# Kernel tuning notes

Hardware: AMD Instinct MI355X
Metric: run time of the kernel (lower is better)

The kernel has to match this reference:

```python
import math
import jax, jax.numpy as jnp
import numpy as np

H = 16  # head_count
D = 1024  # model_dim
DH = D // H  # dim_per_head = 64
PAD_IDX = 1


def setup_inputs() -> dict:
    key = jax.random.key(0)
    ks = jax.random.split(key, 16)
    B, L = 4, 512
    s = 0.02
    inp = {
        'key': jax.random.normal(ks[0], (B, L, D), jnp.float32),
        'value': jax.random.normal(ks[1], (B, L, D), jnp.float32),
        'query': jax.random.normal(ks[2], (B, L, D), jnp.float32),
        'ast_parents_matrix': jax.random.randint(ks[3], (B, L, L), 0, 200, jnp.int32),
        'mask': jnp.zeros((B, 1, L), jnp.bool_),
        'Wq': jax.random.normal(ks[4], (D, D), jnp.float32) * s,
        'bq': jnp.zeros((D,), jnp.float32),
        'Wk': jax.random.normal(ks[5], (D, D), jnp.float32) * s,
        'bk': jnp.zeros((D,), jnp.float32),
        'Wv': jax.random.normal(ks[6], (D, D), jnp.float32) * s,
        'bv': jnp.zeros((D,), jnp.float32),
        'Wo': jax.random.normal(ks[7], (D, D), jnp.float32) * s,
        'bo': jnp.zeros((D,), jnp.float32),
        'struct_emb': jax.random.normal(ks[8], (200, DH), jnp.float32).at[PAD_IDX].set(0.0),
        'value_emb': jax.random.normal(ks[9], (10000, DH), jnp.float32).at[PAD_IDX].set(0.0),
    }
    return inp


def _parent_embeddings(matrix, struct_emb, value_emb):
    # matrix: (B, Lq, K) int ids; even key positions use structure vocab, odd use value vocab
    B, Lq, K = matrix.shape
    s_ids = matrix[:, :, ::2]   # (B, Lq, ceil(K/2))
    v_ids = matrix[:, :, 1::2]  # (B, Lq, floor(K/2))
    emb_s = struct_emb[s_ids]   # (B, Lq, S, DH)
    emb_v = value_emb[v_ids]    # (B, Lq, V, DH)
    S = emb_s.shape[2]
    if emb_v.shape[2] != S:  # odd K: pad value stream by one zero slot, drop after interleave
        emb_v = jnp.concatenate([emb_v, jnp.zeros_like(emb_s[:, :, :1])], axis=2)
    pe = jnp.stack([emb_s, emb_v], axis=3).reshape(B, Lq, 2 * S, DH)
    return pe[:, :, :K, :]  # (B, Lq, K, DH)


def reference(key, value, query, ast_parents_matrix, mask,
              Wq, bq, Wk, bk, Wv, bv, Wo, bo, struct_emb, value_emb):
    B, L, _ = query.shape

    def shape(x):
        return x.reshape(B, -1, H, DH).transpose(0, 2, 1, 3)  # (B,H,L,DH)

    q = shape(query @ Wq + bq) / math.sqrt(DH)
    k = shape(key @ Wk + bk)
    v = shape(value @ Wv + bv)

    qk = jnp.einsum('bhid,bhjd->bhij', q, k)  # (B,H,L,L)

    pe = _parent_embeddings(ast_parents_matrix[:, :, :L], struct_emb, value_emb)
    score_ast = jnp.einsum('bhid,bijd->bhij', q, pe)

    scores = (qk + score_ast).astype(jnp.float32)
    scores = jnp.where(mask[:, None, :, :], -1e18, scores)  # mask: (B,1,L)->(B,1,1,L)
    attn = jax.nn.softmax(scores, axis=-1).astype(q.dtype)
    # dropout p=0.0 (eval) -> identity
    context = jnp.einsum('bhij,bhjd->bhid', attn, v)  # (B,H,L,DH)
    context = context.transpose(0, 2, 1, 3).reshape(B, L, D)
    output = context @ Wo + bo
    return output, attn
```

## Files before the change

### kernel.cpp

```cpp
#include <hip/hip_runtime.h>
#include <cstddef>

#define H 16
#define D 1024
#define DH 64
#define L 512

typedef __attribute__((ext_vector_type(8))) short bf16x8;
typedef __attribute__((ext_vector_type(4))) short bf16x4;
typedef __attribute__((ext_vector_type(4))) float f32x4;

__device__ inline short f2bf(float x) {
    union { float f; unsigned u; } c; c.f = x;
    unsigned r = (c.u + 0x7FFFu + ((c.u >> 16) & 1u)) >> 16;
    return (short)r;
}
__device__ inline float bf2f(short x) {
    union { float f; unsigned u; } c;
    c.u = ((unsigned)(unsigned short)x) << 16; return c.f;
}

__device__ inline void gload_lds16(const void* g, void* l) {
    __builtin_amdgcn_global_load_lds(
        (const __attribute__((address_space(1))) unsigned int*)g,
        (__attribute__((address_space(3))) unsigned int*)l,
        16, 0, 0);
}

struct PrepArgs {
    const float* csrc[5]; short* cdst[5]; int cn[5];
    const float* W[4]; short* T[4];
};

__global__ __launch_bounds__(256) void prep_kernel(PrepArgs a) {
    const int y = blockIdx.y;
    if (y < 5) {
        const float* s = a.csrc[y];
        short* d = a.cdst[y];
        int n = a.cn[y];
        int i = (blockIdx.x * 256 + threadIdx.x) * 8;
        if (i >= n) return;
        float4 x0 = *(const float4*)(s + i);
        float4 x1 = *(const float4*)(s + i + 4);
        bf16x8 o;
        o[0] = f2bf(x0.x); o[1] = f2bf(x0.y); o[2] = f2bf(x0.z); o[3] = f2bf(x0.w);
        o[4] = f2bf(x1.x); o[5] = f2bf(x1.y); o[6] = f2bf(x1.z); o[7] = f2bf(x1.w);
        *(bf16x8*)(d + i) = o;
    } else {
        const float* W = a.W[y - 5];
        short* T = a.T[y - 5];
        int idx = blockIdx.x * 256 + threadIdx.x;
        if (idx >= 1024 * 128) return;
        int n = idx & 1023;
        int k0 = (idx >> 10) << 3;
        bf16x8 o;
        #pragma unroll
        for (int kk = 0; kk < 8; ++kk)
            o[kk] = f2bf(W[(size_t)(k0 + kk) * 1024 + n]);
        *(bf16x8*)(T + (size_t)n * 1024 + k0) = o;
    }
}

#define BM 128
#define BN 64
#define BKK 64

struct GemmBatch {
    const short* A[3]; const short* Bt[3]; const float* bias[3];
    void* out[3]; float scale[3]; int mode[3];
};

__global__ __launch_bounds__(256) void gemm_mfma_kernel(GemmBatch P, int M, int N, int K) {
    const int z = blockIdx.z;
    const short* __restrict__ A  = P.A[z];
    const short* __restrict__ Bt = P.Bt[z];
    const float* __restrict__ bias = P.bias[z];
    const float scale = P.scale[z];
    const int mode = P.mode[z];

    __shared__ short lds[(BM + BN) * BKK];
    short* As = lds;
    short* Bs = lds + BM * BKK;

    const int tid = threadIdx.x;
    const int wave = tid >> 6, lane = tid & 63;
    const int fm = lane & 15, quad = lane >> 4;
    const int m0 = blockIdx.y * BM, n0 = blockIdx.x * BN;

    int arow[4], acol[4];
    #pragma unroll
    for (int t = 0; t < 4; ++t) {
        int s = (wave * 4 + t) * 64 + lane;
        int row = s >> 3;
        int u = (s & 7) ^ (row & 7);
        arow[t] = row; acol[t] = u * 8;
    }
    int brow[2], bcol[2];
    #pragma unroll
    for (int t = 0; t < 2; ++t) {
        int s = (wave * 2 + t) * 64 + lane;
        int row = s >> 3;
        int u = (s & 7) ^ (row & 7);
        brow[t] = row; bcol[t] = u * 8;
    }

    int aoff[2][2], boff[4][2];
    #pragma unroll
    for (int mt = 0; mt < 2; ++mt)
        #pragma unroll
        for (int kst = 0; kst < 2; ++kst) {
            int row = wave * 32 + mt * 16 + fm;
            int u = quad + 4 * kst;
            aoff[mt][kst] = row * 64 + ((u ^ (row & 7)) * 8);
        }
    #pragma unroll
    for (int nt = 0; nt < 4; ++nt)
        #pragma unroll
        for (int kst = 0; kst < 2; ++kst) {
            int row = nt * 16 + fm;
            int u = quad + 4 * kst;
            boff[nt][kst] = row * 64 + ((u ^ (row & 7)) * 8);
        }

    f32x4 acc[2][4];
    #pragma unroll
    for (int mt = 0; mt < 2; ++mt)
        #pragma unroll
        for (int nt = 0; nt < 4; ++nt) acc[mt][nt] = (f32x4){0.f, 0.f, 0.f, 0.f};

    for (int k0 = 0; k0 < K; k0 += BKK) {
        __syncthreads();
        #pragma unroll
        for (int t = 0; t < 4; ++t)
            gload_lds16(A + (size_t)(m0 + arow[t]) * K + k0 + acol[t],
                        As + (wave * 4 + t) * 512);
        #pragma unroll
        for (int t = 0; t < 2; ++t)
            gload_lds16(Bt + (size_t)(n0 + brow[t]) * K + k0 + bcol[t],
                        Bs + (wave * 2 + t) * 512);
        __syncthreads();
        #pragma unroll
        for (int kst = 0; kst < 2; ++kst) {
            bf16x8 af[2], bfr[4];
            af[0] = *(const bf16x8*)(As + aoff[0][kst]);
            af[1] = *(const bf16x8*)(As + aoff[1][kst]);
            #pragma unroll
            for (int nt = 0; nt < 4; ++nt)
                bfr[nt] = *(const bf16x8*)(Bs + boff[nt][kst]);
            #pragma unroll
            for (int mt = 0; mt < 2; ++mt)
                #pragma unroll
                for (int nt = 0; nt < 4; ++nt)
                    acc[mt][nt] = __builtin_amdgcn_mfma_f32_16x16x32_bf16(
                        af[mt], bfr[nt], acc[mt][nt], 0, 0, 0);
        }
    }

    if (mode == 2) {
        __syncthreads();
        short (*T)[BM + 8] = (short(*)[BM + 8])&lds[0];
        #pragma unroll
        for (int mt = 0; mt < 2; ++mt)
            #pragma unroll
            for (int nt = 0; nt < 4; ++nt) {
                int nn = nt * 16 + fm;
                float bv = bias[n0 + nn];
                #pragma unroll
                for (int r = 0; r < 4; ++r) {
                    int mm = wave * 32 + mt * 16 + quad * 4 + r;
                    T[nn][mm] = f2bf((acc[mt][nt][r] + bv) * scale);
                }
            }
        __syncthreads();
        int b = m0 >> 9;
        int ibase = m0 & (L - 1);
        int hblk = n0 >> 6;
        int n = tid >> 2, seg = (tid & 3) * 32;
        short* dst = (short*)P.out[z] + (((size_t)(b * H + hblk) * DH + n) * L) + ibase + seg;
        #pragma unroll
        for (int c = 0; c < 4; ++c)
            *(bf16x8*)(dst + c * 8) = *(const bf16x8*)(&T[n][seg + c * 8]);
    } else {
        #pragma unroll
        for (int mt = 0; mt < 2; ++mt)
            #pragma unroll
            for (int nt = 0; nt < 4; ++nt) {
                int n = n0 + nt * 16 + fm;
                float bv = bias[n];
                #pragma unroll
                for (int r = 0; r < 4; ++r) {
                    int m = m0 + wave * 32 + mt * 16 + quad * 4 + r;
                    float val = (acc[mt][nt][r] + bv) * scale;
                    if (mode == 0) {
                        ((float*)P.out[z])[(size_t)m * N + n] = val;
                    } else {
                        int b = m >> 9, i = m & (L - 1);
                        int h = n >> 6, d = n & (DH - 1);
                        ((short*)P.out[z])[(((size_t)(b * H + h) * L + i) * DH) + d] = f2bf(val);
                    }
                }
            }
    }
}

__global__ __launch_bounds__(256) void ast_kernel(
    const short* __restrict__ Qb, const int* __restrict__ mat,
    const short* __restrict__ semb, const short* __restrict__ vemb,
    short* __restrict__ Sast)
{
    const int i = blockIdx.x, b = blockIdx.y;
    const int tid = threadIdx.x;
    const int wave = tid >> 6, lane = tid & 63;
    const int fm = lane & 15, quad = lane >> 4;
    __shared__ short Sl[H][L + 8];

    const short* qp = Qb + (((size_t)(b * H + fm) * L + i) * DH);
    bf16x8 a0 = *(const bf16x8*)(qp + quad * 8);
    bf16x8 a1 = *(const bf16x8*)(qp + 32 + quad * 8);

    const int* mrow = mat + ((size_t)b * L + i) * L;

    int idxs[8];
    const short* ebase[8];
    #pragma unroll
    for (int t = 0; t < 8; ++t) {
        int j = (wave + t * 4) * 16 + fm;
        idxs[t] = mrow[j];
    }
    #pragma unroll
    for (int t = 0; t < 8; ++t) {
        int j = (wave + t * 4) * 16 + fm;
        ebase[t] = ((j & 1) ? vemb : semb) + (size_t)idxs[t] * DH;
    }

    #pragma unroll
    for (int t = 0; t < 8; ++t) {
        int j = (wave + t * 4) * 16 + fm;
        bf16x8 b0 = *(const bf16x8*)(ebase[t] + quad * 8);
        bf16x8 b1 = *(const bf16x8*)(ebase[t] + 32 + quad * 8);
        f32x4 c = {0.f, 0.f, 0.f, 0.f};
        c = __builtin_amdgcn_mfma_f32_16x16x32_bf16(a0, b0, c, 0, 0, 0);
        c = __builtin_amdgcn_mfma_f32_16x16x32_bf16(a1, b1, c, 0, 0, 0);
        #pragma unroll
        for (int r = 0; r < 4; ++r)
            Sl[quad * 4 + r][j] = f2bf(c[r]);
    }
    __syncthreads();
    int hh = tid >> 4, j0 = (tid & 15) * 32;
    short* dst = Sast + ((((size_t)b * L + i) * H + hh) * L) + j0;
    #pragma unroll
    for (int c = 0; c < 4; ++c)
        *(bf16x8*)(dst + c * 8) = *(const bf16x8*)(&Sl[hh][j0 + c * 8]);
}

__global__ __launch_bounds__(256, 3) void attn_fused_kernel(
    const short* __restrict__ Qb, const short* __restrict__ Kb,
    const short* __restrict__ Vt, const short* __restrict__ Sast,
    const unsigned char* __restrict__ mask,
    float* __restrict__ attn, short* __restrict__ ctx)
{
    const int i0 = blockIdx.x * 16;
    const int h = blockIdx.y;
    const int b = blockIdx.z;
    const int tid = threadIdx.x;
    const int wave = tid >> 6, lane = tid & 63;
    const int fm = lane & 15, quad = lane >> 4;
    const int jw = wave * 128;

    __shared__ short Pl[16][520];
    __shared__ float red_m[4][16];
    __shared__ float red_l[4][16];

    const short* qp = Qb + (((size_t)(b * H + h) * L + i0 + fm) * DH);
    bf16x8 q0 = *(const bf16x8*)(qp + quad * 8);
    bf16x8 q1 = *(const bf16x8*)(qp + 32 + quad * 8);
    const short* Kbase = Kb + ((size_t)(b * H + h) * L) * DH;
    const short* sastrow = Sast + (((size_t)b * L + i0 + fm) * H + h) * L;
    const unsigned char* mrow = mask + (size_t)b * L + jw;

    bf16x8 kf0[8], kf1[8];
    bf16x4 sa[8];
    unsigned mku[8];
    #pragma unroll
    for (int t = 0; t < 8; ++t) {
        const short* kr = Kbase + (size_t)(jw + t * 16 + fm) * DH;
        kf0[t] = *(const bf16x8*)(kr + quad * 8);
        kf1[t] = *(const bf16x8*)(kr + 32 + quad * 8);
        sa[t]  = *(const bf16x4*)(sastrow + jw + t * 16 + quad * 4);
        mku[t] = *(const unsigned*)(mrow + t * 16 + quad * 4);
    }
    __builtin_amdgcn_sched_barrier(0);

    float s[8][4];
    float mx = -3.0e38f;
    #pragma unroll
    for (int t = 0; t < 8; ++t) {
        f32x4 c = {0.f, 0.f, 0.f, 0.f};
        c = __builtin_amdgcn_mfma_f32_16x16x32_bf16(kf0[t], q0, c, 0, 0, 0);
        c = __builtin_amdgcn_mfma_f32_16x16x32_bf16(kf1[t], q1, c, 0, 0, 0);
        #pragma unroll
        for (int r = 0; r < 4; ++r) {
            float sv = c[r] + bf2f(sa[t][r]);
            sv = ((mku[t] >> (8 * r)) & 255u) ? -1e18f : sv;
            s[t][r] = sv;
            mx = fmaxf(mx, sv);
        }
    }

    bf16x8 vf[16];
    const short* Vb = Vt + (((size_t)(b * H + h) * DH + wave * 16 + fm) * L);
    #pragma unroll
    for (int i = 0; i < 16; ++i)
        vf[i] = *(const bf16x8*)(Vb + i * 32 + quad * 8);
    __builtin_amdgcn_sched_barrier(0);

    mx = fmaxf(mx, __shfl_xor(mx, 16));
    mx = fmaxf(mx, __shfl_xor(mx, 32));

    float sum = 0.f;
    #pragma unroll
    for (int t = 0; t < 8; ++t)
        #pragma unroll
        for (int r = 0; r < 4; ++r) {
            float e = __expf(s[t][r] - mx);
            s[t][r] = e;
            sum += e;
        }
    sum += __shfl_xor(sum, 16);
    sum += __shfl_xor(sum, 32);
    if (quad == 0) {
        red_m[wave][fm] = mx;
        red_l[wave][fm] = sum;
    }
    __syncthreads();

    float m0_ = red_m[0][fm], m1_ = red_m[1][fm];
    float m2_ = red_m[2][fm], m3_ = red_m[3][fm];
    float M_ = fmaxf(fmaxf(m0_, m1_), fmaxf(m2_, m3_));
    float T_ = red_l[0][fm] * __expf(m0_ - M_)
             + red_l[1][fm] * __expf(m1_ - M_)
             + red_l[2][fm] * __expf(m2_ - M_)
             + red_l[3][fm] * __expf(m3_ - M_);
    float fac = __expf(mx - M_) / T_;

    float* arow = attn + (((size_t)(b * H + h) * L + i0 + fm) * L);
    #pragma unroll
    for (int t = 0; t < 8; ++t) {
        int jt = jw + t * 16 + quad * 4;
        bf16x4 pw;
        #pragma unroll
        for (int r = 0; r < 4; ++r)
            pw[r] = f2bf(s[t][r] * fac);
        *(bf16x4*)(&Pl[fm][jt]) = pw;
        float4 v;
        v.x = bf2f(pw[0]); v.y = bf2f(pw[1]); v.z = bf2f(pw[2]); v.w = bf2f(pw[3]);
        *(float4*)(arow + jt) = v;
    }
    __syncthreads();

    f32x4 o = {0.f, 0.f, 0.f, 0.f};
    #pragma unroll
    for (int ks = 0; ks < 16; ++ks) {
        bf16x8 pa = *(const bf16x8*)(&Pl[fm][ks * 32 + quad * 8]);
        o = __builtin_amdgcn_mfma_f32_16x16x32_bf16(pa, vf[ks], o, 0, 0, 0);
    }
    #pragma unroll
    for (int r = 0; r < 4; ++r)
        ctx[((size_t)b * L + i0 + quad * 4 + r) * D + h * DH + wave * 16 + fm] = f2bf(o[r]);
}

extern "C" void kernel_launch(void* const* d_in, const int* in_sizes, int n_in,
                              void* d_out, int out_size, void* d_ws, size_t ws_size,
                              hipStream_t stream) {
    const float* key_in   = (const float*)d_in[0];
    const float* value_in = (const float*)d_in[1];
    const float* query_in = (const float*)d_in[2];
    const int*   mat      = (const int*)d_in[3];
    const unsigned char* mask = (const unsigned char*)d_in[4];
    const float* Wq = (const float*)d_in[5];
    const float* bq = (const float*)d_in[6];
    const float* Wk = (const float*)d_in[7];
    const float* bk = (const float*)d_in[8];
    const float* Wv = (const float*)d_in[9];
    const float* bv = (const float*)d_in[10];
    const float* Wo = (const float*)d_in[11];
    const float* bo = (const float*)d_in[12];
    const float* struct_emb = (const float*)d_in[13];
    const float* value_emb  = (const float*)d_in[14];

    const int B = in_sizes[2] / (L * D);
    const int M = B * L;

    short* p = (short*)d_ws;
    short* xk  = p;  p += (size_t)M * D;
    short* xv  = p;  p += (size_t)M * D;
    short* xq  = p;  p += (size_t)M * D;
    short* WqT = p;  p += (size_t)D * D;
    short* WkT = p;  p += (size_t)D * D;
    short* WvT = p;  p += (size_t)D * D;
    short* WoT = p;  p += (size_t)D * D;
    short* semb = p; p += 16384;
    short* vemb = p; p += (size_t)in_sizes[14];
    short* Qb = p;   p += (size_t)M * D;
    short* Kb = p;   p += (size_t)M * D;
    short* Vt = p;   p += (size_t)M * D;
    short* Sast = p; p += (size_t)B * L * H * L;
    short* ctx = xk;

    float* out_p  = (float*)d_out;
    float* attn_p = out_p + (size_t)M * D;

    PrepArgs pa;
    pa.csrc[0] = key_in;     pa.cdst[0] = xk;   pa.cn[0] = M * D;
    pa.csrc[1] = value_in;   pa.cdst[1] = xv;   pa.cn[1] = M * D;
    pa.csrc[2] = query_in;   pa.cdst[2] = xq;   pa.cn[2] = M * D;
    pa.csrc[3] = struct_emb; pa.cdst[3] = semb; pa.cn[3] = in_sizes[13];
    pa.csrc[4] = value_emb;  pa.cdst[4] = vemb; pa.cn[4] = in_sizes[14];
    pa.W[0] = Wq; pa.W[1] = Wk; pa.W[2] = Wv; pa.W[3] = Wo;
    pa.T[0] = WqT; pa.T[1] = WkT; pa.T[2] = WvT; pa.T[3] = WoT;
    prep_kernel<<<dim3((M * D) / 2048, 9), 256, 0, stream>>>(pa);

    GemmBatch qkv;
    qkv.A[0] = xq; qkv.Bt[0] = WqT; qkv.bias[0] = bq; qkv.out[0] = Qb; qkv.scale[0] = 0.125f; qkv.mode[0] = 1;
    qkv.A[1] = xk; qkv.Bt[1] = WkT; qkv.bias[1] = bk; qkv.out[1] = Kb; qkv.scale[1] = 1.0f;   qkv.mode[1] = 1;
    qkv.A[2] = xv; qkv.Bt[2] = WvT; qkv.bias[2] = bv; qkv.out[2] = Vt; qkv.scale[2] = 1.0f;   qkv.mode[2] = 2;
    gemm_mfma_kernel<<<dim3(D / BN, M / BM, 3), 256, 0, stream>>>(qkv, M, D, D);

    ast_kernel<<<dim3(L, B), 256, 0, stream>>>(Qb, mat, semb, vemb, Sast);

    attn_fused_kernel<<<dim3(L / 16, H, B), 256, 0, stream>>>(
        Qb, Kb, Vt, Sast, mask, attn_p, ctx);

    GemmBatch fin;
    fin.A[0] = ctx; fin.Bt[0] = WoT; fin.bias[0] = bo; fin.out[0] = out_p; fin.scale[0] = 1.0f; fin.mode[0] = 0;
    fin.A[1] = ctx; fin.Bt[1] = WoT; fin.bias[1] = bo; fin.out[1] = out_p; fin.scale[1] = 1.0f; fin.mode[1] = 0;
    fin.A[2] = ctx; fin.Bt[2] = WoT; fin.bias[2] = bo; fin.out[2] = out_p; fin.scale[2] = 1.0f; fin.mode[2] = 0;
    gemm_mfma_kernel<<<dim3(D / BN, M / BM, 1), 256, 0, stream>>>(fin, M, D, D);
}
```

Measured before the change: 241.6 us.

## Stage K and V through swizzled LDS and remap blocks per XCD

```diff
diff --git a/kernel.cpp b/kernel.cpp
--- a/kernel.cpp
+++ b/kernel.cpp
@@ -253,67 +253,87 @@
         *(bf16x8*)(dst + c * 8) = *(const bf16x8*)(&Sl[hh][j0 + c * 8]);
 }
 
-__global__ __launch_bounds__(256, 3) void attn_fused_kernel(
+#define PPI 520
+
+__global__ __launch_bounds__(256) void attn_fused_kernel(
     const short* __restrict__ Qb, const short* __restrict__ Kb,
     const short* __restrict__ Vt, const short* __restrict__ Sast,
     const unsigned char* __restrict__ mask,
     float* __restrict__ attn, short* __restrict__ ctx)
 {
-    const int i0 = blockIdx.x * 16;
-    const int h = blockIdx.y;
-    const int b = blockIdx.z;
+    const int flat = blockIdx.x + (blockIdx.y << 5) + (blockIdx.z << 9);
+    const int xcd = flat & 7;
+    const int slot = flat >> 3;
+    const int pair = ((slot >> 5) << 3) + xcd;
+    const int i0 = (slot & 31) * 16;
+    const int h = pair & 15;
+    const int b = pair >> 4;
+
     const int tid = threadIdx.x;
     const int wave = tid >> 6, lane = tid & 63;
     const int fm = lane & 15, quad = lane >> 4;
     const int jw = wave * 128;
 
-    __shared__ short Pl[16][520];
+    __shared__ short Ks[512 * 64];
+    __shared__ short Vs[64 * 512];
+    __shared__ short Pl[16][PPI];
     __shared__ float red_m[4][16];
     __shared__ float red_l[4][16];
+
+    const short* Kbase = Kb + ((size_t)(b * H + h) * L) * DH;
+    const short* Vbase = Vt + ((size_t)(b * H + h) * DH) * L;
+
+    #pragma unroll
+    for (int p = 0; p < 16; ++p) {
+        int s = p * 256 + tid;
+        int row = s >> 3;
+        int u = (s & 7) ^ (row & 7);
+        gload_lds16(Kbase + (size_t)row * 64 + u * 8,
+                    Ks + (p * 256 + wave * 64) * 8);
+    }
+    #pragma unroll
+    for (int p = 0; p < 16; ++p) {
+        int s = p * 256 + tid;
+        int row = s >> 6;
+        int c = (s & 63) ^ (row & 7);
+        gload_lds16(Vbase + (size_t)row * 512 + c * 8,
+                    Vs + (p * 256 + wave * 64) * 8);
+    }
 
     const short* qp = Qb + (((size_t)(b * H + h) * L + i0 + fm) * DH);
     bf16x8 q0 = *(const bf16x8*)(qp + quad * 8);
     bf16x8 q1 = *(const bf16x8*)(qp + 32 + quad * 8);
-    const short* Kbase = Kb + ((size_t)(b * H + h) * L) * DH;
     const short* sastrow = Sast + (((size_t)b * L + i0 + fm) * H + h) * L;
     const unsigned char* mrow = mask + (size_t)b * L + jw;
-
-    bf16x8 kf0[8], kf1[8];
     bf16x4 sa[8];
     unsigned mku[8];
     #pragma unroll
     for (int t = 0; t < 8; ++t) {
-        const short* kr = Kbase + (size_t)(jw + t * 16 + fm) * DH;
-        kf0[t] = *(const bf16x8*)(kr + quad * 8);
-        kf1[t] = *(const bf16x8*)(kr + 32 + quad * 8);
         sa[t]  = *(const bf16x4*)(sastrow + jw + t * 16 + quad * 4);
         mku[t] = *(const unsigned*)(mrow + t * 16 + quad * 4);
     }
-    __builtin_amdgcn_sched_barrier(0);
-
-    float s[8][4];
+
+    __syncthreads();
+
+    float s_[8][4];
     float mx = -3.0e38f;
     #pragma unroll
     for (int t = 0; t < 8; ++t) {
+        int j = jw + t * 16 + fm;
+        bf16x8 k0 = *(const bf16x8*)(Ks + j * 64 + ((quad ^ (j & 7)) * 8));
+        bf16x8 k1 = *(const bf16x8*)(Ks + j * 64 + (((quad + 4) ^ (j & 7)) * 8));
         f32x4 c = {0.f, 0.f, 0.f, 0.f};
-        c = __builtin_amdgcn_mfma_f32_16x16x32_bf16(kf0[t], q0, c, 0, 0, 0);
-        c = __builtin_amdgcn_mfma_f32_16x16x32_bf16(kf1[t], q1, c, 0, 0, 0);
+        c = __builtin_amdgcn_mfma_f32_16x16x32_bf16(k0, q0, c, 0, 0, 0);
+        c = __builtin_amdgcn_mfma_f32_16x16x32_bf16(k1, q1, c, 0, 0, 0);
         #pragma unroll
         for (int r = 0; r < 4; ++r) {
             float sv = c[r] + bf2f(sa[t][r]);
             sv = ((mku[t] >> (8 * r)) & 255u) ? -1e18f : sv;
-            s[t][r] = sv;
+            s_[t][r] = sv;
             mx = fmaxf(mx, sv);
         }
     }
 
-    bf16x8 vf[16];
-    const short* Vb = Vt + (((size_t)(b * H + h) * DH + wave * 16 + fm) * L);
-    #pragma unroll
-    for (int i = 0; i < 16; ++i)
-        vf[i] = *(const bf16x8*)(Vb + i * 32 + quad * 8);
-    __builtin_amdgcn_sched_barrier(0);
-
     mx = fmaxf(mx, __shfl_xor(mx, 16));
     mx = fmaxf(mx, __shfl_xor(mx, 32));
 
@@ -322,8 +342,8 @@
     for (int t = 0; t < 8; ++t)
         #pragma unroll
         for (int r = 0; r < 4; ++r) {
-            float e = __expf(s[t][r] - mx);
-            s[t][r] = e;
+            float e = __expf(s_[t][r] - mx);
+            s_[t][r] = e;
             sum += e;
         }
     sum += __shfl_xor(sum, 16);
@@ -350,7 +370,7 @@
         bf16x4 pw;
         #pragma unroll
         for (int r = 0; r < 4; ++r)
-            pw[r] = f2bf(s[t][r] * fac);
+            pw[r] = f2bf(s_[t][r] * fac);
         *(bf16x4*)(&Pl[fm][jt]) = pw;
         float4 v;
         v.x = bf2f(pw[0]); v.y = bf2f(pw[1]); v.z = bf2f(pw[2]); v.w = bf2f(pw[3]);
@@ -361,8 +381,11 @@
     f32x4 o = {0.f, 0.f, 0.f, 0.f};
     #pragma unroll
     for (int ks = 0; ks < 16; ++ks) {
+        int row = wave * 16 + fm;
+        int c = ((ks * 4) + quad) ^ (row & 7);
         bf16x8 pa = *(const bf16x8*)(&Pl[fm][ks * 32 + quad * 8]);
-        o = __builtin_amdgcn_mfma_f32_16x16x32_bf16(pa, vf[ks], o, 0, 0, 0);
+        bf16x8 vb = *(const bf16x8*)(Vs + row * 512 + c * 8);
+        o = __builtin_amdgcn_mfma_f32_16x16x32_bf16(pa, vb, o, 0, 0, 0);
     }
     #pragma unroll
     for (int r = 0; r < 4; ++r)
```

Measured after the change: 244.0 us. Within noise of the previous version (+1.0%).
